# Kernel optimization log

Hardware: AMD Instinct MI355X
Metric: run time of the kernel (lower is better)

Reference implementation:

```python
import jax, jax.numpy as jnp
import numpy as np

N_NODES = 50000
N_EDGES = 800000
D_IN = 96
D_HID = 96
D_OUT = 96


def _mean_agg(x, src, dst, n_nodes):
    # mean over in-neighbors: agg[v] = mean_{(u->v) in E} x[u]
    msg = x[src]  # [E, d] irregular gather
    summed = jax.ops.segment_sum(msg, dst, num_segments=n_nodes)  # [N, d]
    deg = jax.ops.segment_sum(jnp.ones((src.shape[0],), x.dtype), dst,
                              num_segments=n_nodes)  # [N]
    return summed / jnp.maximum(deg, 1.0)[:, None]


def _sage_conv(x, src, dst, W_self, W_neigh, b):
    agg = _mean_agg(x, src, dst, x.shape[0])
    return x @ W_self + agg @ W_neigh + b


def setup_inputs() -> dict:
    key = jax.random.key(0)
    ks = jax.random.split(key, 9)
    s = 0.05
    return {
        "x": jax.random.normal(ks[0], (N_NODES, D_IN), jnp.float32),
        "src": jax.random.randint(ks[1], (N_EDGES,), 0, N_NODES),
        "dst": jax.random.randint(ks[2], (N_EDGES,), 0, N_NODES),
        "W_self1": jax.random.normal(ks[3], (D_IN, D_HID), jnp.float32) * s,
        "W_neigh1": jax.random.normal(ks[4], (D_IN, D_HID), jnp.float32) * s,
        "b1": jnp.zeros((D_HID,), jnp.float32),
        "W_self2": jax.random.normal(ks[5], (D_HID, D_OUT), jnp.float32) * s,
        "W_neigh2": jax.random.normal(ks[6], (D_HID, D_OUT), jnp.float32) * s,
        "b2": jnp.zeros((D_OUT,), jnp.float32),
    }


def reference(x, src, dst, W_self1, W_neigh1, b1, W_self2, W_neigh2, b2):
    h = _sage_conv(x, src, dst, W_self1, W_neigh1, b1)
    h = jax.nn.relu(h)
    h = _sage_conv(h, src, dst, W_self2, W_neigh2, b2)
    return h
```

## Files before the change

### kernel.cpp

```cpp
#include <hip/hip_runtime.h>
#include <cstdint>
#include <cstddef>

#define NN 50000
#define NE 800000
#define D 96

#define NBUCK 512
#define BSH 7
#define NBU ((NN + 127) >> 7)
#define TILE 8192
#define NTILE ((NE + TILE - 1) / TILE)
#define MAXB 5120

#define AGB 32
#define AGW 1024

typedef __attribute__((ext_vector_type(8))) short bf16x8;
typedef __attribute__((ext_vector_type(4))) float f32x4;


__global__ void init_cur(int* __restrict__ bucketCur) {
    bucketCur[threadIdx.x] = (int)threadIdx.x * MAXB;
}

__launch_bounds__(512)
__global__ void bin_edges(const int* __restrict__ dst, const int* __restrict__ src,
                          int* __restrict__ bucketCur, uint2* __restrict__ pairBuf) {
    __shared__ int hist[NBUCK];
    __shared__ int segStart[NBUCK];
    __shared__ int lcur[NBUCK];
    __shared__ int segBase[NBUCK];
    __shared__ uint2 lpair[TILE];
    const int t = threadIdx.x;
    const int e0 = blockIdx.x * TILE;
    const int cnt = (NE - e0 < TILE) ? (NE - e0) : TILE;

    for (int i = t; i < NBUCK; i += 512) hist[i] = 0;
    __syncthreads();

    for (int i = t * 4; i < cnt; i += 512 * 4) {
        if (i + 3 < cnt) {
            int4 d4 = *(const int4*)(dst + e0 + i);
            atomicAdd(&hist[d4.x >> BSH], 1);
            atomicAdd(&hist[d4.y >> BSH], 1);
            atomicAdd(&hist[d4.z >> BSH], 1);
            atomicAdd(&hist[d4.w >> BSH], 1);
        } else {
            for (int k = i; k < cnt; ++k) atomicAdd(&hist[dst[e0 + k] >> BSH], 1);
        }
    }
    __syncthreads();

    {
        const int v = hist[t];
        segStart[t] = v;
        __syncthreads();
        for (int s = 1; s < NBUCK; s <<= 1) {
            int u = (t >= s) ? segStart[t - s] : 0;
            __syncthreads();
            segStart[t] += u;
            __syncthreads();
        }
        int excl = segStart[t] - v;
        __syncthreads();
        segStart[t] = excl;
        lcur[t] = excl;
    }
    __syncthreads();

    for (int i = t * 4; i < cnt; i += 512 * 4) {
        if (i + 3 < cnt) {
            int4 d4 = *(const int4*)(dst + e0 + i);
            int4 s4 = *(const int4*)(src + e0 + i);
            int p0 = atomicAdd(&lcur[d4.x >> BSH], 1); lpair[p0] = make_uint2(d4.x, s4.x);
            int p1 = atomicAdd(&lcur[d4.y >> BSH], 1); lpair[p1] = make_uint2(d4.y, s4.y);
            int p2 = atomicAdd(&lcur[d4.z >> BSH], 1); lpair[p2] = make_uint2(d4.z, s4.z);
            int p3 = atomicAdd(&lcur[d4.w >> BSH], 1); lpair[p3] = make_uint2(d4.w, s4.w);
        } else {
            for (int k = i; k < cnt; ++k) {
                int d = dst[e0 + k], s = src[e0 + k];
                int p = atomicAdd(&lcur[d >> BSH], 1);
                lpair[p] = make_uint2(d, s);
            }
        }
    }
    __syncthreads();

    {
        int c = hist[t];
        segBase[t] = c ? atomicAdd(&bucketCur[t], c) : 0;
    }
    __syncthreads();

    for (int k = t; k < cnt; k += 512) {
        uint2 p = lpair[k];
        int b = (int)p.x >> BSH;
        pairBuf[(size_t)segBase[b] + (k - segStart[b])] = p;
    }
}

__global__ void csr_build(const uint2* __restrict__ pairBuf, const int* __restrict__ bucketCur,
                          int* __restrict__ deg, int* __restrict__ startv,
                          int* __restrict__ csr) {
    __shared__ int h[128], ls[128], cur[128];
    __shared__ int lsrc[MAXB];
    const int b = blockIdx.x;
    const int t = threadIdx.x;
    const int lo = b * MAXB;
    int cnt = bucketCur[b] - lo;
    if (cnt > MAXB) cnt = MAXB;
    const int node0 = b << BSH;

    if (t < 128) h[t] = 0;
    __syncthreads();
    for (int k = t; k < cnt; k += 256)
        atomicAdd(&h[(int)pairBuf[lo + k].x - node0], 1);
    __syncthreads();
    if (t < 128) ls[t] = h[t];
    __syncthreads();
    for (int s = 1; s < 128; s <<= 1) {
        int u = (t >= s && t < 128) ? ls[t - s] : 0;
        __syncthreads();
        if (t < 128) ls[t] += u;
        __syncthreads();
    }
    if (t < 128) {
        int excl = ls[t] - h[t];
        cur[t] = excl;
        int node = node0 + t;
        if (node < NN) {
            deg[node] = h[t];
            startv[node] = lo + excl;
        }
    }
    __syncthreads();
    for (int k = t; k < cnt; k += 256) {
        uint2 p = pairBuf[lo + k];
        int pos = atomicAdd(&cur[(int)p.x - node0], 1);
        lsrc[pos] = (int)p.y;
    }
    __syncthreads();
    for (int k = t; k < cnt; k += 256) csr[lo + k] = lsrc[k];
}


__device__ inline uint32_t pack2_bf16(float a, float b) {
    uint32_t ua = __float_as_uint(a), ub = __float_as_uint(b);
    ua = (ua + 0x7fffu + ((ua >> 16) & 1u)) >> 16;
    ub = (ub + 0x7fffu + ((ub >> 16) & 1u)) >> 16;
    return ua | (ub << 16);
}

__device__ inline unsigned short pack1_bf16(float a) {
    uint32_t ua = __float_as_uint(a);
    return (unsigned short)((ua + 0x7fffu + ((ua >> 16) & 1u)) >> 16);
}

__device__ inline float bf_lo(uint32_t w) { return __uint_as_float(w << 16); }
__device__ inline float bf_hi(uint32_t w) { return __uint_as_float(w & 0xffff0000u); }


__global__ void repack_both(const float* __restrict__ Ws1, const float* __restrict__ Wn1,
                            const float* __restrict__ Ws2, const float* __restrict__ Wn2,
                            uint32_t* __restrict__ bfg1, uint32_t* __restrict__ bfg2) {
    int t = blockIdx.x * 256 + threadIdx.x;
    if (t >= 4608) return;
    const int layer = (t >= 2304);
    int tt = t - layer * 2304;
    const int isWn = (tt >= 1152);
    const float* __restrict__ W = layer ? (isWn ? Wn2 : Ws2) : (isWn ? Wn1 : Ws1);
    uint32_t* __restrict__ Bfg = layer ? bfg2 : bfg1;
    tt = isWn ? tt - 1152 : tt;
    int s = tt / 384;
    int r = tt - s * 384;
    int nt6 = r >> 6;
    int l = r & 63;
    int col = nt6 * 16 + (l & 15);
    int k0 = 32 * s + 8 * (l >> 4);
    float v[8];
#pragma unroll
    for (int j = 0; j < 8; ++j) v[j] = W[(k0 + j) * D + col];
    uint4 o;
    o.x = pack2_bf16(v[0], v[1]);
    o.y = pack2_bf16(v[2], v[3]);
    o.z = pack2_bf16(v[4], v[5]);
    o.w = pack2_bf16(v[6], v[7]);
    int nt = nt6 + (isWn ? 6 : 0);
    int slot = (s * 12 + nt) * 64 + l;
    *(uint4*)(Bfg + (size_t)slot * 4) = o;
}


__launch_bounds__(256, 2)
__global__ void xform1_mfma(const float* __restrict__ X,
                            const uint32_t* __restrict__ Bfg,
                            const float* __restrict__ Bias,
                            unsigned short* __restrict__ Ys,
                            unsigned short* __restrict__ Yn) {
    __shared__ __align__(16) uint32_t Af[64 * 52];
    const int tid = threadIdx.x;
    const int row0 = blockIdx.x * 64;

#pragma unroll
    for (int it = 0; it < 6; ++it) {
        int flat = (it * 256 + tid) * 4;
        int r = flat / 96, k = flat - (flat / 96) * 96;
        int gr = row0 + r;
        if (gr >= NN) gr = NN - 1;
        float4 xv = *(const float4*)(X + (size_t)gr * D + k);
        int wq = r >> 4, s = k >> 5;
        int lq = ((k >> 3) & 3) * 16 + (r & 15);
        int base = ((wq * 3 + s) * 64 + lq) * 4 + ((k & 7) >> 1);
        Af[base] = pack2_bf16(xv.x, xv.y);
        Af[base + 1] = pack2_bf16(xv.z, xv.w);
    }
    __syncthreads();

    const int w = tid >> 6, l = tid & 63;
    const int cl = l & 15;

    bf16x8 a0 = *(const bf16x8*)&Af[((w * 3 + 0) * 64 + l) * 4];
    bf16x8 a1 = *(const bf16x8*)&Af[((w * 3 + 1) * 64 + l) * 4];
    bf16x8 a2 = *(const bf16x8*)&Af[((w * 3 + 2) * 64 + l) * 4];

    f32x4 acc[12];
#pragma unroll
    for (int nt = 0; nt < 6; ++nt) {
        float bv = Bias[nt * 16 + cl];
        acc[nt] = (f32x4){bv, bv, bv, bv};
    }
#pragma unroll
    for (int nt = 6; nt < 12; ++nt) acc[nt] = (f32x4){0.f, 0.f, 0.f, 0.f};

#pragma unroll
    for (int nt = 0; nt < 12; ++nt) {
        bf16x8 b0 = *(const bf16x8*)(Bfg + ((size_t)((0 * 12 + nt) * 64 + l)) * 4);
        bf16x8 b1 = *(const bf16x8*)(Bfg + ((size_t)((1 * 12 + nt) * 64 + l)) * 4);
        bf16x8 b2 = *(const bf16x8*)(Bfg + ((size_t)((2 * 12 + nt) * 64 + l)) * 4);
        acc[nt] = __builtin_amdgcn_mfma_f32_16x16x32_bf16(a0, b0, acc[nt], 0, 0, 0);
        acc[nt] = __builtin_amdgcn_mfma_f32_16x16x32_bf16(a1, b1, acc[nt], 0, 0, 0);
        acc[nt] = __builtin_amdgcn_mfma_f32_16x16x32_bf16(a2, b2, acc[nt], 0, 0, 0);
    }
    __syncthreads();

    unsigned short* Af16 = (unsigned short*)Af;
    const int lrow = w * 16 + (l >> 4) * 4;

#pragma unroll
    for (int nt = 0; nt < 6; ++nt)
#pragma unroll
        for (int rg = 0; rg < 4; ++rg)
            Af16[(lrow + rg) * 104 + nt * 16 + cl] = pack1_bf16(acc[nt][rg]);
    __syncthreads();
    {
        uint32_t* Ysu = (uint32_t*)Ys;
        const int rowq = tid >> 2, colq = (tid & 3) * 12;
        if (row0 + rowq < NN) {
#pragma unroll
            for (int i = 0; i < 3; ++i)
                *(uint4*)(Ysu + (size_t)(row0 + rowq) * 48 + colq + i * 4) =
                    *(const uint4*)&Af[rowq * 52 + colq + i * 4];
        }
    }
    __syncthreads();

#pragma unroll
    for (int nt = 6; nt < 12; ++nt)
#pragma unroll
        for (int rg = 0; rg < 4; ++rg)
            Af16[(lrow + rg) * 104 + (nt - 6) * 16 + cl] = pack1_bf16(acc[nt][rg]);
    __syncthreads();
    {
        uint32_t* Ynu = (uint32_t*)Yn;
        const int rowq = tid >> 2, colq = (tid & 3) * 12;
        if (row0 + rowq < NN) {
#pragma unroll
            for (int i = 0; i < 3; ++i)
                *(uint4*)(Ynu + (size_t)(row0 + rowq) * 48 + colq + i * 4) =
                    *(const uint4*)&Af[rowq * 52 + colq + i * 4];
        }
    }
}


#define GATHER_BODY(TBL, GET)                                              \
    {                                                                      \
        int e = 0;                                                         \
        for (; e + 15 < dg; e += 16) {                                     \
            uint32_t wv[16];                                               \
            _Pragma("unroll")                                              \
            for (int i = 0; i < 16; ++i)                                   \
                wv[i] = TBL[(size_t)(GET(e + i)) * 48 + li];               \
            _Pragma("unroll")                                              \
            for (int i = 0; i < 16; ++i) {                                 \
                sx[i & 3] += bf_lo(wv[i]); sy[i & 3] += bf_hi(wv[i]);      \
            }                                                              \
        }                                                                  \
        if (e + 7 < dg) {                                                  \
            uint32_t wv[8];                                                \
            _Pragma("unroll")                                              \
            for (int i = 0; i < 8; ++i)                                    \
                wv[i] = TBL[(size_t)(GET(e + i)) * 48 + li];               \
            _Pragma("unroll")                                              \
            for (int i = 0; i < 8; ++i) {                                  \
                sx[i & 3] += bf_lo(wv[i]); sy[i & 3] += bf_hi(wv[i]);      \
            }                                                              \
            e += 8;                                                        \
        }                                                                  \
        if (e + 3 < dg) {                                                  \
            uint32_t wv[4];                                                \
            _Pragma("unroll")                                              \
            for (int i = 0; i < 4; ++i)                                    \
                wv[i] = TBL[(size_t)(GET(e + i)) * 48 + li];               \
            _Pragma("unroll")                                              \
            for (int i = 0; i < 4; ++i) {                                  \
                sx[i] += bf_lo(wv[i]); sy[i] += bf_hi(wv[i]);              \
            }                                                              \
            e += 4;                                                        \
        }                                                                  \
        for (; e < dg; ++e) {                                              \
            uint32_t wv = TBL[(size_t)(GET(e)) * 48 + li];                 \
            sx[0] += bf_lo(wv); sy[0] += bf_hi(wv);                        \
        }                                                                  \
    }


__launch_bounds__(256, 4)
__global__ void fused_aggx(const unsigned short* __restrict__ Ys1,
                           const uint32_t* __restrict__ Yn1,
                           const int* __restrict__ csr, const int* __restrict__ startv,
                           const int* __restrict__ deg, const int* __restrict__ bucketCur,
                           const uint32_t* __restrict__ Bfg2, const float* __restrict__ Bias2,
                           unsigned short* __restrict__ Ys2, unsigned short* __restrict__ Yn2) {
    __shared__ __align__(16) uint32_t H[AGB * 52];
    __shared__ __align__(16) uint32_t H2[AGB * 52];
    __shared__ int lcsr[AGW];
    __shared__ int lsv[AGB + 1];
    __shared__ int ldeg[AGB];
    const int tid = threadIdx.x;
    const int w = tid >> 6, l = tid & 63;
    const int row0 = blockIdx.x * AGB;
    const int li = (l < 48) ? l : 0;

    if (tid <= AGB) {
        int r = row0 + tid;
        lsv[tid] = (r < NN) ? startv[r] : bucketCur[NBU - 1];
    }
    if (tid < AGB) {
        int r = row0 + tid;
        ldeg[tid] = (r < NN) ? deg[r] : 0;
    }
    __syncthreads();
    const int e_lo = lsv[0];
    const int wcnt = lsv[AGB] - e_lo;
    const int staged = wcnt < AGW ? wcnt : AGW;
    for (int k = tid; k < staged; k += 256) lcsr[k] = csr[e_lo + k];
    __syncthreads();

    for (int j = 0; j < 8; ++j) {
        const int vl = w * 8 + j;
        const int v = row0 + vl;
        uint32_t hpair = 0;
        if (v < NN) {
            const int sloc = lsv[vl] - e_lo;
            const int dg = ldeg[vl];
            float sx[4], sy[4];
#pragma unroll
            for (int i = 0; i < 4; ++i) { sx[i] = 0.f; sy[i] = 0.f; }
            if (sloc + dg <= staged) {
#define GET_L(E) lcsr[sloc + (E)]
                GATHER_BODY(Yn1, GET_L)
#undef GET_L
            } else {
                const int* cp = csr + e_lo + sloc;
#define GET_G(E) cp[E]
                GATHER_BODY(Yn1, GET_G)
#undef GET_G
            }
            float ax = (sx[0] + sx[1]) + (sx[2] + sx[3]);
            float ay = (sy[0] + sy[1]) + (sy[2] + sy[3]);
            const float inv = 1.f / (float)(dg > 0 ? dg : 1);
            uint32_t ysp = *(const uint32_t*)(Ys1 + (size_t)v * 96 + 2 * li);
            float r0 = fmaxf(bf_lo(ysp) + ax * inv, 0.f);
            float r1 = fmaxf(bf_hi(ysp) + ay * inv, 0.f);
            hpair = pack2_bf16(r0, r1);
        }
        if (l < 48) H[vl * 52 + l] = hpair;
    }
    __syncthreads();

    const int stripe = w >> 1;
    const int hf = w & 1;
    const int cl = l & 15;
    const int kq = l >> 4;

    bf16x8 a0 = *(const bf16x8*)&H[(stripe * 16 + cl) * 52 + 0 + 4 * kq];
    bf16x8 a1 = *(const bf16x8*)&H[(stripe * 16 + cl) * 52 + 16 + 4 * kq];
    bf16x8 a2 = *(const bf16x8*)&H[(stripe * 16 + cl) * 52 + 32 + 4 * kq];

    f32x4 acc[6];
#pragma unroll
    for (int nt = 0; nt < 6; ++nt) {
        float bv = hf ? 0.f : Bias2[nt * 16 + cl];
        acc[nt] = (f32x4){bv, bv, bv, bv};
    }
#pragma unroll
    for (int nt = 0; nt < 6; ++nt) {
        int ntg = hf * 6 + nt;
        bf16x8 b0 = *(const bf16x8*)(Bfg2 + ((size_t)((0 * 12 + ntg) * 64 + l)) * 4);
        bf16x8 b1 = *(const bf16x8*)(Bfg2 + ((size_t)((1 * 12 + ntg) * 64 + l)) * 4);
        bf16x8 b2 = *(const bf16x8*)(Bfg2 + ((size_t)((2 * 12 + ntg) * 64 + l)) * 4);
        acc[nt] = __builtin_amdgcn_mfma_f32_16x16x32_bf16(a0, b0, acc[nt], 0, 0, 0);
        acc[nt] = __builtin_amdgcn_mfma_f32_16x16x32_bf16(a1, b1, acc[nt], 0, 0, 0);
        acc[nt] = __builtin_amdgcn_mfma_f32_16x16x32_bf16(a2, b2, acc[nt], 0, 0, 0);
    }
    __syncthreads();

    {
        unsigned short* Hb = (unsigned short*)(hf ? H2 : H);
        const int lrow = stripe * 16 + kq * 4;
#pragma unroll
        for (int nt = 0; nt < 6; ++nt)
#pragma unroll
            for (int rg = 0; rg < 4; ++rg)
                Hb[(lrow + rg) * 104 + nt * 16 + cl] = pack1_bf16(acc[nt][rg]);
    }
    __syncthreads();

    {
        const int row = tid >> 3, colq = (tid & 7) * 6;
        if (row0 + row < NN) {
            uint32_t* Ysu = (uint32_t*)Ys2;
            uint32_t* Ynu = (uint32_t*)Yn2;
            const size_t gb = (size_t)(row0 + row) * 48 + colq;
            const int lb = row * 52 + colq;
#pragma unroll
            for (int i = 0; i < 3; ++i)
                *(uint2*)(Ysu + gb + i * 2) = *(const uint2*)&H[lb + i * 2];
#pragma unroll
            for (int i = 0; i < 3; ++i)
                *(uint2*)(Ynu + gb + i * 2) = *(const uint2*)&H2[lb + i * 2];
        }
    }
}


__launch_bounds__(256, 4)
__global__ void agg_final(const unsigned short* __restrict__ Ys2b,
                          const uint32_t* __restrict__ Yn2,
                          const int* __restrict__ csr, const int* __restrict__ startv,
                          const int* __restrict__ deg, const int* __restrict__ bucketCur,
                          float* __restrict__ out) {
    __shared__ int lcsr[AGW];
    __shared__ int lsv[AGB + 1];
    __shared__ int ldeg[AGB];
    const int tid = threadIdx.x;
    const int w = tid >> 6, l = tid & 63;
    const int row0 = blockIdx.x * AGB;
    const int li = (l < 48) ? l : 0;

    if (tid <= AGB) {
        int r = row0 + tid;
        lsv[tid] = (r < NN) ? startv[r] : bucketCur[NBU - 1];
    }
    if (tid < AGB) {
        int r = row0 + tid;
        ldeg[tid] = (r < NN) ? deg[r] : 0;
    }
    __syncthreads();
    const int e_lo = lsv[0];
    const int wcnt = lsv[AGB] - e_lo;
    const int staged = wcnt < AGW ? wcnt : AGW;
    for (int k = tid; k < staged; k += 256) lcsr[k] = csr[e_lo + k];
    __syncthreads();

    for (int j = 0; j < 8; ++j) {
        const int vl = w * 8 + j;
        const int v = row0 + vl;
        if (v >= NN) continue;
        const int sloc = lsv[vl] - e_lo;
        const int dg = ldeg[vl];
        float sx[4], sy[4];
#pragma unroll
        for (int i = 0; i < 4; ++i) { sx[i] = 0.f; sy[i] = 0.f; }
        if (sloc + dg <= staged) {
#define GET_L(E) lcsr[sloc + (E)]
            GATHER_BODY(Yn2, GET_L)
#undef GET_L
        } else {
            const int* cp = csr + e_lo + sloc;
#define GET_G(E) cp[E]
            GATHER_BODY(Yn2, GET_G)
#undef GET_G
        }
        float ax = (sx[0] + sx[1]) + (sx[2] + sx[3]);
        float ay = (sy[0] + sy[1]) + (sy[2] + sy[3]);
        const float inv = 1.f / (float)(dg > 0 ? dg : 1);
        if (l < 48) {
            const size_t o = (size_t)v * D + 2 * li;
            uint32_t ysp = *(const uint32_t*)(Ys2b + (size_t)v * 96 + 2 * li);
            out[o] = bf_lo(ysp) + ax * inv;
            out[o + 1] = bf_hi(ysp) + ay * inv;
        }
    }
}


extern "C" void kernel_launch(void* const* d_in, const int* in_sizes, int n_in,
                              void* d_out, int out_size, void* d_ws, size_t ws_size,
                              hipStream_t stream) {
    const float* x   = (const float*)d_in[0];
    const int*   src = (const int*)d_in[1];
    const int*   dst = (const int*)d_in[2];
    const float* Ws1 = (const float*)d_in[3];
    const float* Wn1 = (const float*)d_in[4];
    const float* b1  = (const float*)d_in[5];
    const float* Ws2 = (const float*)d_in[6];
    const float* Wn2 = (const float*)d_in[7];
    const float* b2  = (const float*)d_in[8];
    float* out = (float*)d_out;

    char* w = (char*)d_ws;
    int* startv    = (int*)w; w += (size_t)NN * sizeof(int);
    int* deg       = (int*)w; w += (size_t)NN * sizeof(int);
    int* bucketCur = (int*)w; w += NBUCK * sizeof(int);
    int* csr       = (int*)w; w += (size_t)NBUCK * MAXB * sizeof(int);
    w = (char*)(((uintptr_t)w + 255) & ~(uintptr_t)255);
    unsigned short* ys1 = (unsigned short*)w; w += (size_t)NN * D * sizeof(unsigned short);
    unsigned short* yn1 = (unsigned short*)w; w += (size_t)NN * D * sizeof(unsigned short);
    unsigned short* ys2 = (unsigned short*)w; w += (size_t)NN * D * sizeof(unsigned short);
    unsigned short* yn2 = (unsigned short*)w; w += (size_t)NN * D * sizeof(unsigned short);
    uint32_t* bfg1 = (uint32_t*)w; w += 36 * 64 * 4 * sizeof(uint32_t);
    uint32_t* bfg2 = (uint32_t*)w; w += 36 * 64 * 4 * sizeof(uint32_t);

    uint2* pairBuf = (uint2*)ys1;

    init_cur<<<1, NBUCK, 0, stream>>>(bucketCur);
    bin_edges<<<NTILE, 512, 0, stream>>>(dst, src, bucketCur, pairBuf);
    csr_build<<<NBU, 256, 0, stream>>>(pairBuf, bucketCur, deg, startv, csr);

    repack_both<<<18, 256, 0, stream>>>(Ws1, Wn1, Ws2, Wn2, bfg1, bfg2);

    xform1_mfma<<<(NN + 63) / 64, 256, 0, stream>>>(x, bfg1, b1, ys1, yn1);

    const int agrid = (NN + AGB - 1) / AGB;

    fused_aggx<<<agrid, 256, 0, stream>>>(ys1, (const uint32_t*)yn1, csr, startv, deg,
                                          bucketCur, bfg2, b2, ys2, yn2);

    agg_final<<<agrid, 256, 0, stream>>>(ys2, (const uint32_t*)yn2, csr, startv, deg,
                                         bucketCur, out);
}
```

Before: 114.4 us.

## Split neighbor gathers by source half to improve L2 locality

Each node's CSR neighbor list is partitioned by whether the source index falls in the lower or upper half of the node range, and the aggregation kernels run two passes, first over lower-half sources and then over upper-half sources, keeping partial sums in shared memory. The goal is to shrink the working set of gathered feature rows in each pass so it fits better in cache. The change also folds the bucket-cursor init into the weight repack kernel, saving a launch. It drops the second staging buffer in fused_aggx and raises launch-bounds occupancy hints, at the cost of serialized output writes, a large float accumulator array in shared memory, and extra syncs.

Result: slower. 128.3 us (+12.1%).

```diff
diff --git a/kernel.cpp b/kernel.cpp
--- a/kernel.cpp
+++ b/kernel.cpp
@@ -5,6 +5,7 @@
 #define NN 50000
 #define NE 800000
 #define D 96
+#define NSPLIT 25000
 
 #define NBUCK 512
 #define BSH 7
@@ -19,10 +20,6 @@
 typedef __attribute__((ext_vector_type(8))) short bf16x8;
 typedef __attribute__((ext_vector_type(4))) float f32x4;
 
-
-__global__ void init_cur(int* __restrict__ bucketCur) {
-    bucketCur[threadIdx.x] = (int)threadIdx.x * MAXB;
-}
 
 __launch_bounds__(512)
 __global__ void bin_edges(const int* __restrict__ dst, const int* __restrict__ src,
@@ -102,8 +99,8 @@
 
 __global__ void csr_build(const uint2* __restrict__ pairBuf, const int* __restrict__ bucketCur,
                           int* __restrict__ deg, int* __restrict__ startv,
-                          int* __restrict__ csr) {
-    __shared__ int h[128], ls[128], cur[128];
+                          int* __restrict__ splitv, int* __restrict__ csr) {
+    __shared__ int h[256], ls[256], cur[256];
     __shared__ int lsrc[MAXB];
     const int b = blockIdx.x;
     const int t = threadIdx.x;
@@ -112,32 +109,39 @@
     if (cnt > MAXB) cnt = MAXB;
     const int node0 = b << BSH;
 
-    if (t < 128) h[t] = 0;
-    __syncthreads();
-    for (int k = t; k < cnt; k += 256)
-        atomicAdd(&h[(int)pairBuf[lo + k].x - node0], 1);
-    __syncthreads();
-    if (t < 128) ls[t] = h[t];
-    __syncthreads();
-    for (int s = 1; s < 128; s <<= 1) {
-        int u = (t >= s && t < 128) ? ls[t - s] : 0;
+    h[t] = 0;
+    __syncthreads();
+    for (int k = t; k < cnt; k += 256) {
+        uint2 p = pairBuf[lo + k];
+        atomicAdd(&h[((int)p.x - node0) * 2 + ((int)p.y >= NSPLIT)], 1);
+    }
+    __syncthreads();
+    ls[t] = h[t];
+    __syncthreads();
+    for (int s = 1; s < 256; s <<= 1) {
+        int u = (t >= s) ? ls[t - s] : 0;
         __syncthreads();
-        if (t < 128) ls[t] += u;
+        ls[t] += u;
         __syncthreads();
     }
-    if (t < 128) {
+    {
         int excl = ls[t] - h[t];
         cur[t] = excl;
-        int node = node0 + t;
+        int node = node0 + (t >> 1);
         if (node < NN) {
-            deg[node] = h[t];
-            startv[node] = lo + excl;
+            if ((t & 1) == 0) {
+                deg[node] = h[t] + h[t + 1];
+                startv[node] = lo + excl;
+            } else {
+                splitv[node] = lo + excl;
+            }
         }
     }
     __syncthreads();
     for (int k = t; k < cnt; k += 256) {
         uint2 p = pairBuf[lo + k];
-        int pos = atomicAdd(&cur[(int)p.x - node0], 1);
+        int key = ((int)p.x - node0) * 2 + ((int)p.y >= NSPLIT);
+        int pos = atomicAdd(&cur[key], 1);
         lsrc[pos] = (int)p.y;
     }
     __syncthreads();
@@ -161,9 +165,16 @@
 __device__ inline float bf_hi(uint32_t w) { return __uint_as_float(w & 0xffff0000u); }
 
 
-__global__ void repack_both(const float* __restrict__ Ws1, const float* __restrict__ Wn1,
+__global__ void repack_init(const float* __restrict__ Ws1, const float* __restrict__ Wn1,
                             const float* __restrict__ Ws2, const float* __restrict__ Wn2,
-                            uint32_t* __restrict__ bfg1, uint32_t* __restrict__ bfg2) {
+                            uint32_t* __restrict__ bfg1, uint32_t* __restrict__ bfg2,
+                            int* __restrict__ bucketCur) {
+    if (blockIdx.x == 18) {
+        int t = threadIdx.x;
+        bucketCur[t] = t * MAXB;
+        bucketCur[t + 256] = (t + 256) * MAXB;
+        return;
+    }
     int t = blockIdx.x * 256 + threadIdx.x;
     if (t >= 4608) return;
     const int layer = (t >= 2304);
@@ -325,18 +336,31 @@
         }                                                                  \
     }
 
-
-__launch_bounds__(256, 4)
+#define PASS_GATHER(TBL)                                                   \
+    if (sloc + dg <= staged) {                                             \
+        GATHER_BODY(TBL, GET_L)                                            \
+    } else {                                                               \
+        const int* cp = csr + e_lo + sloc;                                 \
+        GATHER_BODY(TBL, GET_G)                                            \
+    }
+
+#define GET_L(E) lcsr[sloc + (E)]
+#define GET_G(E) cp[E]
+
+
+__launch_bounds__(256, 6)
 __global__ void fused_aggx(const unsigned short* __restrict__ Ys1,
                            const uint32_t* __restrict__ Yn1,
                            const int* __restrict__ csr, const int* __restrict__ startv,
-                           const int* __restrict__ deg, const int* __restrict__ bucketCur,
+                           const int* __restrict__ splitv, const int* __restrict__ deg,
+                           const int* __restrict__ bucketCur,
                            const uint32_t* __restrict__ Bfg2, const float* __restrict__ Bias2,
                            unsigned short* __restrict__ Ys2, unsigned short* __restrict__ Yn2) {
+    __shared__ float accF[AGB][100];
     __shared__ __align__(16) uint32_t H[AGB * 52];
-    __shared__ __align__(16) uint32_t H2[AGB * 52];
     __shared__ int lcsr[AGW];
     __shared__ int lsv[AGB + 1];
+    __shared__ int lsp[AGB];
     __shared__ int ldeg[AGB];
     const int tid = threadIdx.x;
     const int w = tid >> 6, l = tid & 63;
@@ -349,6 +373,7 @@
     }
     if (tid < AGB) {
         int r = row0 + tid;
+        lsp[tid] = (r < NN) ? splitv[r] : 0;
         ldeg[tid] = (r < NN) ? deg[r] : 0;
     }
     __syncthreads();
@@ -358,35 +383,38 @@
     for (int k = tid; k < staged; k += 256) lcsr[k] = csr[e_lo + k];
     __syncthreads();
 
-    for (int j = 0; j < 8; ++j) {
-        const int vl = w * 8 + j;
-        const int v = row0 + vl;
-        uint32_t hpair = 0;
-        if (v < NN) {
-            const int sloc = lsv[vl] - e_lo;
-            const int dg = ldeg[vl];
-            float sx[4], sy[4];
-#pragma unroll
-            for (int i = 0; i < 4; ++i) { sx[i] = 0.f; sy[i] = 0.f; }
-            if (sloc + dg <= staged) {
-#define GET_L(E) lcsr[sloc + (E)]
-                GATHER_BODY(Yn1, GET_L)
-#undef GET_L
-            } else {
-                const int* cp = csr + e_lo + sloc;
-#define GET_G(E) cp[E]
-                GATHER_BODY(Yn1, GET_G)
-#undef GET_G
+    for (int p = 0; p < 2; ++p) {
+        for (int j = 0; j < 8; ++j) {
+            const int vl = w * 8 + j;
+            const int v = row0 + vl;
+            if (v < NN) {
+                const int s0 = lsv[vl] - e_lo;
+                const int sp = lsp[vl] - e_lo;
+                const int dgA = ldeg[vl];
+                const int sloc = p ? sp : s0;
+                const int dg = p ? (s0 + dgA - sp) : (sp - s0);
+                float sx[4], sy[4];
+#pragma unroll
+                for (int i = 0; i < 4; ++i) { sx[i] = 0.f; sy[i] = 0.f; }
+                PASS_GATHER(Yn1)
+                float ax = (sx[0] + sx[1]) + (sx[2] + sx[3]);
+                float ay = (sy[0] + sy[1]) + (sy[2] + sy[3]);
+                if (p == 0) {
+                    accF[vl][2 * li] = ax;
+                    accF[vl][2 * li + 1] = ay;
+                } else {
+                    ax += accF[vl][2 * li];
+                    ay += accF[vl][2 * li + 1];
+                    const float inv = 1.f / (float)(dgA > 0 ? dgA : 1);
+                    uint32_t ysp = *(const uint32_t*)(Ys1 + (size_t)v * 96 + 2 * li);
+                    float r0 = fmaxf(bf_lo(ysp) + ax * inv, 0.f);
+                    float r1 = fmaxf(bf_hi(ysp) + ay * inv, 0.f);
+                    if (l < 48) H[vl * 52 + l] = pack2_bf16(r0, r1);
+                }
+            } else if (p == 1 && l < 48) {
+                H[vl * 52 + l] = 0;
             }
-            float ax = (sx[0] + sx[1]) + (sx[2] + sx[3]);
-            float ay = (sy[0] + sy[1]) + (sy[2] + sy[3]);
-            const float inv = 1.f / (float)(dg > 0 ? dg : 1);
-            uint32_t ysp = *(const uint32_t*)(Ys1 + (size_t)v * 96 + 2 * li);
-            float r0 = fmaxf(bf_lo(ysp) + ax * inv, 0.f);
-            float r1 = fmaxf(bf_hi(ysp) + ay * inv, 0.f);
-            hpair = pack2_bf16(r0, r1);
-        }
-        if (l < 48) H[vl * 52 + l] = hpair;
+        }
     }
     __syncthreads();
 
@@ -418,42 +446,66 @@
     __syncthreads();
 
     {
-        unsigned short* Hb = (unsigned short*)(hf ? H2 : H);
+        unsigned short* Hb = (unsigned short*)H;
         const int lrow = stripe * 16 + kq * 4;
-#pragma unroll
-        for (int nt = 0; nt < 6; ++nt)
-#pragma unroll
-            for (int rg = 0; rg < 4; ++rg)
-                Hb[(lrow + rg) * 104 + nt * 16 + cl] = pack1_bf16(acc[nt][rg]);
-    }
-    __syncthreads();
-
+        if (hf == 0) {
+#pragma unroll
+            for (int nt = 0; nt < 6; ++nt)
+#pragma unroll
+                for (int rg = 0; rg < 4; ++rg)
+                    Hb[(lrow + rg) * 104 + nt * 16 + cl] = pack1_bf16(acc[nt][rg]);
+        }
+    }
+    __syncthreads();
     {
         const int row = tid >> 3, colq = (tid & 7) * 6;
         if (row0 + row < NN) {
             uint32_t* Ysu = (uint32_t*)Ys2;
+            const size_t gb = (size_t)(row0 + row) * 48 + colq;
+            const int lb = row * 52 + colq;
+#pragma unroll
+            for (int i = 0; i < 3; ++i)
+                *(uint2*)(Ysu + gb + i * 2) = *(const uint2*)&H[lb + i * 2];
+        }
+    }
+    __syncthreads();
+
+    {
+        unsigned short* Hb = (unsigned short*)H;
+        const int lrow = stripe * 16 + kq * 4;
+        if (hf == 1) {
+#pragma unroll
+            for (int nt = 0; nt < 6; ++nt)
+#pragma unroll
+                for (int rg = 0; rg < 4; ++rg)
+                    Hb[(lrow + rg) * 104 + nt * 16 + cl] = pack1_bf16(acc[nt][rg]);
+        }
+    }
+    __syncthreads();
+    {
+        const int row = tid >> 3, colq = (tid & 7) * 6;
+        if (row0 + row < NN) {
             uint32_t* Ynu = (uint32_t*)Yn2;
             const size_t gb = (size_t)(row0 + row) * 48 + colq;
             const int lb = row * 52 + colq;
 #pragma unroll
             for (int i = 0; i < 3; ++i)
-                *(uint2*)(Ysu + gb + i * 2) = *(const uint2*)&H[lb + i * 2];
-#pragma unroll
-            for (int i = 0; i < 3; ++i)
-                *(uint2*)(Ynu + gb + i * 2) = *(const uint2*)&H2[lb + i * 2];
-        }
-    }
-}
-
-
-__launch_bounds__(256, 4)
+                *(uint2*)(Ynu + gb + i * 2) = *(const uint2*)&H[lb + i * 2];
+        }
+    }
+}
+
+
+__launch_bounds__(256, 8)
 __global__ void agg_final(const unsigned short* __restrict__ Ys2b,
                           const uint32_t* __restrict__ Yn2,
                           const int* __restrict__ csr, const int* __restrict__ startv,
-                          const int* __restrict__ deg, const int* __restrict__ bucketCur,
-                          float* __restrict__ out) {
+                          const int* __restrict__ splitv, const int* __restrict__ deg,
+                          const int* __restrict__ bucketCur, float* __restrict__ out) {
+    __shared__ float accF[AGB][100];
     __shared__ int lcsr[AGW];
     __shared__ int lsv[AGB + 1];
+    __shared__ int lsp[AGB];
     __shared__ int ldeg[AGB];
     const int tid = threadIdx.x;
     const int w = tid >> 6, l = tid & 63;
@@ -466,6 +518,7 @@
     }
     if (tid < AGB) {
         int r = row0 + tid;
+        lsp[tid] = (r < NN) ? splitv[r] : 0;
         ldeg[tid] = (r < NN) ? deg[r] : 0;
     }
     __syncthreads();
@@ -475,33 +528,34 @@
     for (int k = tid; k < staged; k += 256) lcsr[k] = csr[e_lo + k];
     __syncthreads();
 
-    for (int j = 0; j < 8; ++j) {
-        const int vl = w * 8 + j;
-        const int v = row0 + vl;
-        if (v >= NN) continue;
-        const int sloc = lsv[vl] - e_lo;
-        const int dg = ldeg[vl];
-        float sx[4], sy[4];
-#pragma unroll
-        for (int i = 0; i < 4; ++i) { sx[i] = 0.f; sy[i] = 0.f; }
-        if (sloc + dg <= staged) {
-#define GET_L(E) lcsr[sloc + (E)]
-            GATHER_BODY(Yn2, GET_L)
-#undef GET_L
-        } else {
-            const int* cp = csr + e_lo + sloc;
-#define GET_G(E) cp[E]
-            GATHER_BODY(Yn2, GET_G)
-#undef GET_G
-        }
-        float ax = (sx[0] + sx[1]) + (sx[2] + sx[3]);
-        float ay = (sy[0] + sy[1]) + (sy[2] + sy[3]);
-        const float inv = 1.f / (float)(dg > 0 ? dg : 1);
-        if (l < 48) {
-            const size_t o = (size_t)v * D + 2 * li;
-            uint32_t ysp = *(const uint32_t*)(Ys2b + (size_t)v * 96 + 2 * li);
-            out[o] = bf_lo(ysp) + ax * inv;
-            out[o + 1] = bf_hi(ysp) + ay * inv;
+    for (int p = 0; p < 2; ++p) {
+        for (int j = 0; j < 8; ++j) {
+            const int vl = w * 8 + j;
+            const int v = row0 + vl;
+            if (v >= NN) continue;
+            const int s0 = lsv[vl] - e_lo;
+            const int sp = lsp[vl] - e_lo;
+            const int dgA = ldeg[vl];
+            const int sloc = p ? sp : s0;
+            const int dg = p ? (s0 + dgA - sp) : (sp - s0);
+            float sx[4], sy[4];
+#pragma unroll
+            for (int i = 0; i < 4; ++i) { sx[i] = 0.f; sy[i] = 0.f; }
+            PASS_GATHER(Yn2)
+            float ax = (sx[0] + sx[1]) + (sx[2] + sx[3]);
+            float ay = (sy[0] + sy[1]) + (sy[2] + sy[3]);
+            if (p == 0) {
+                accF[vl][2 * li] = ax;
+                accF[vl][2 * li + 1] = ay;
+            } else if (l < 48) {
+                ax += accF[vl][2 * li];
+                ay += accF[vl][2 * li + 1];
+                const float inv = 1.f / (float)(dgA > 0 ? dgA : 1);
+                const size_t o = (size_t)v * D + 2 * li;
+                uint32_t ysp = *(const uint32_t*)(Ys2b + (size_t)v * 96 + 2 * li);
+                out[o] = bf_lo(ysp) + ax * inv;
+                out[o + 1] = bf_hi(ysp) + ay * inv;
+            }
         }
     }
 }
@@ -523,6 +577,7 @@
 
     char* w = (char*)d_ws;
     int* startv    = (int*)w; w += (size_t)NN * sizeof(int);
+    int* splitv    = (int*)w; w += (size_t)NN * sizeof(int);
     int* deg       = (int*)w; w += (size_t)NN * sizeof(int);
     int* bucketCur = (int*)w; w += NBUCK * sizeof(int);
     int* csr       = (int*)w; w += (size_t)NBUCK * MAXB * sizeof(int);
@@ -536,19 +591,18 @@
 
     uint2* pairBuf = (uint2*)ys1;
 
-    init_cur<<<1, NBUCK, 0, stream>>>(bucketCur);
+    repack_init<<<19, 256, 0, stream>>>(Ws1, Wn1, Ws2, Wn2, bfg1, bfg2, bucketCur);
+
     bin_edges<<<NTILE, 512, 0, stream>>>(dst, src, bucketCur, pairBuf);
-    csr_build<<<NBU, 256, 0, stream>>>(pairBuf, bucketCur, deg, startv, csr);
-
-    repack_both<<<18, 256, 0, stream>>>(Ws1, Wn1, Ws2, Wn2, bfg1, bfg2);
+    csr_build<<<NBU, 256, 0, stream>>>(pairBuf, bucketCur, deg, startv, splitv, csr);
 
     xform1_mfma<<<(NN + 63) / 64, 256, 0, stream>>>(x, bfg1, b1, ys1, yn1);
 
     const int agrid = (NN + AGB - 1) / AGB;
 
-    fused_aggx<<<agrid, 256, 0, stream>>>(ys1, (const uint32_t*)yn1, csr, startv, deg,
-                                          bucketCur, bfg2, b2, ys2, yn2);
-
-    agg_final<<<agrid, 256, 0, stream>>>(ys2, (const uint32_t*)yn2, csr, startv, deg,
-                                         bucketCur, out);
-}
+    fused_aggx<<<agrid, 256, 0, stream>>>(ys1, (const uint32_t*)yn1, csr, startv, splitv,
+                                          deg, bucketCur, bfg2, b2, ys2, yn2);
+
+    agg_final<<<agrid, 256, 0, stream>>>(ys2, (const uint32_t*)yn2, csr, startv, splitv,
+                                         deg, bucketCur, out);
+}
```

## Software-pipeline neighbor gathers across nodes and merge init into repack kernel

Applied to the files above, without the earlier changes.

Both aggregation kernels are restructured so that the first 16 neighbor-row loads for the next node are issued before the current node's loads are accumulated. Tail edges are handled by clamped indices and masked FMAs instead of branchy remainder loops. The aim is more memory-level parallelism in the latency-bound irregular gather. fused_aggx also drops the second shared-memory buffer and writes Ys2 and Yn2 in two passes through one buffer, which saves LDS to help occupancy at the cost of extra syncs. The bucket-cursor init is folded into the weight repack kernel to remove one launch. The risks are redundant loads for low-degree nodes and higher register pressure from the double buffers.

Measured after the change: 125.1 us. 9.3% more time.

```diff
diff --git a/kernel.cpp b/kernel.cpp
--- a/kernel.cpp
+++ b/kernel.cpp
@@ -19,10 +19,6 @@
 typedef __attribute__((ext_vector_type(8))) short bf16x8;
 typedef __attribute__((ext_vector_type(4))) float f32x4;
 
-
-__global__ void init_cur(int* __restrict__ bucketCur) {
-    bucketCur[threadIdx.x] = (int)threadIdx.x * MAXB;
-}
 
 __launch_bounds__(512)
 __global__ void bin_edges(const int* __restrict__ dst, const int* __restrict__ src,
@@ -161,9 +157,16 @@
 __device__ inline float bf_hi(uint32_t w) { return __uint_as_float(w & 0xffff0000u); }
 
 
-__global__ void repack_both(const float* __restrict__ Ws1, const float* __restrict__ Wn1,
+__global__ void repack_init(const float* __restrict__ Ws1, const float* __restrict__ Wn1,
                             const float* __restrict__ Ws2, const float* __restrict__ Wn2,
-                            uint32_t* __restrict__ bfg1, uint32_t* __restrict__ bfg2) {
+                            uint32_t* __restrict__ bfg1, uint32_t* __restrict__ bfg2,
+                            int* __restrict__ bucketCur) {
+    if (blockIdx.x == 18) {
+        int t = threadIdx.x;
+        bucketCur[t] = t * MAXB;
+        bucketCur[t + 256] = (t + 256) * MAXB;
+        return;
+    }
     int t = blockIdx.x * 256 + threadIdx.x;
     if (t >= 4608) return;
     const int layer = (t >= 2304);
@@ -284,45 +287,44 @@
 }
 
 
-#define GATHER_BODY(TBL, GET)                                              \
-    {                                                                      \
-        int e = 0;                                                         \
-        for (; e + 15 < dg; e += 16) {                                     \
-            uint32_t wv[16];                                               \
-            _Pragma("unroll")                                              \
-            for (int i = 0; i < 16; ++i)                                   \
-                wv[i] = TBL[(size_t)(GET(e + i)) * 48 + li];               \
-            _Pragma("unroll")                                              \
-            for (int i = 0; i < 16; ++i) {                                 \
-                sx[i & 3] += bf_lo(wv[i]); sy[i & 3] += bf_hi(wv[i]);      \
-            }                                                              \
-        }                                                                  \
-        if (e + 7 < dg) {                                                  \
-            uint32_t wv[8];                                                \
-            _Pragma("unroll")                                              \
-            for (int i = 0; i < 8; ++i)                                    \
-                wv[i] = TBL[(size_t)(GET(e + i)) * 48 + li];               \
-            _Pragma("unroll")                                              \
-            for (int i = 0; i < 8; ++i) {                                  \
-                sx[i & 3] += bf_lo(wv[i]); sy[i & 3] += bf_hi(wv[i]);      \
-            }                                                              \
-            e += 8;                                                        \
-        }                                                                  \
-        if (e + 3 < dg) {                                                  \
-            uint32_t wv[4];                                                \
-            _Pragma("unroll")                                              \
-            for (int i = 0; i < 4; ++i)                                    \
-                wv[i] = TBL[(size_t)(GET(e + i)) * 48 + li];               \
-            _Pragma("unroll")                                              \
-            for (int i = 0; i < 4; ++i) {                                  \
-                sx[i] += bf_lo(wv[i]); sy[i] += bf_hi(wv[i]);              \
-            }                                                              \
-            e += 4;                                                        \
-        }                                                                  \
-        for (; e < dg; ++e) {                                              \
-            uint32_t wv = TBL[(size_t)(GET(e)) * 48 + li];                 \
-            sx[0] += bf_lo(wv); sy[0] += bf_hi(wv);                        \
-        }                                                                  \
+#define ISSUE16(TBL, buf, SLOC, DG)                                         \
+    if ((SLOC) + (DG) <= staged) {                                          \
+        _Pragma("unroll")                                                   \
+        for (int i = 0; i < 16; ++i) {                                      \
+            int kk = (i < (DG)) ? i : (DG) - 1;                             \
+            buf[i] = TBL[(size_t)lcsr[(SLOC) + kk] * 48 + li];              \
+        }                                                                   \
+    } else {                                                                \
+        const int* cp_ = csr + e_lo + (SLOC);                               \
+        _Pragma("unroll")                                                   \
+        for (int i = 0; i < 16; ++i) {                                      \
+            int kk = (i < (DG)) ? i : (DG) - 1;                             \
+            buf[i] = TBL[(size_t)cp_[kk] * 48 + li];                        \
+        }                                                                   \
+    }
+
+#define ISSUE16R(TBL, buf, SLOC, DG, E0)                                    \
+    if ((SLOC) + (DG) <= staged) {                                          \
+        _Pragma("unroll")                                                   \
+        for (int i = 0; i < 16; ++i) {                                      \
+            int kk = ((E0) + i < (DG)) ? (E0) + i : (DG) - 1;               \
+            buf[i] = TBL[(size_t)lcsr[(SLOC) + kk] * 48 + li];              \
+        }                                                                   \
+    } else {                                                                \
+        const int* cp_ = csr + e_lo + (SLOC);                               \
+        _Pragma("unroll")                                                   \
+        for (int i = 0; i < 16; ++i) {                                      \
+            int kk = ((E0) + i < (DG)) ? (E0) + i : (DG) - 1;               \
+            buf[i] = TBL[(size_t)cp_[kk] * 48 + li];                        \
+        }                                                                   \
+    }
+
+#define ACC16(buf, DG, E0)                                                  \
+    _Pragma("unroll")                                                       \
+    for (int i = 0; i < 16; ++i) {                                          \
+        float m = ((E0) + i < (DG)) ? 1.f : 0.f;                            \
+        sx[i & 3] = fmaf(m, bf_lo(buf[i]), sx[i & 3]);                      \
+        sy[i & 3] = fmaf(m, bf_hi(buf[i]), sy[i & 3]);                      \
     }
 
 
@@ -334,7 +336,6 @@
                            const uint32_t* __restrict__ Bfg2, const float* __restrict__ Bias2,
                            unsigned short* __restrict__ Ys2, unsigned short* __restrict__ Yn2) {
     __shared__ __align__(16) uint32_t H[AGB * 52];
-    __shared__ __align__(16) uint32_t H2[AGB * 52];
     __shared__ int lcsr[AGW];
     __shared__ int lsv[AGB + 1];
     __shared__ int ldeg[AGB];
@@ -358,36 +359,54 @@
     for (int k = tid; k < staged; k += 256) lcsr[k] = csr[e_lo + k];
     __syncthreads();
 
+    int sl[8], dgj[8];
+#pragma unroll
     for (int j = 0; j < 8; ++j) {
-        const int vl = w * 8 + j;
-        const int v = row0 + vl;
-        uint32_t hpair = 0;
-        if (v < NN) {
-            const int sloc = lsv[vl] - e_lo;
-            const int dg = ldeg[vl];
-            float sx[4], sy[4];
-#pragma unroll
-            for (int i = 0; i < 4; ++i) { sx[i] = 0.f; sy[i] = 0.f; }
-            if (sloc + dg <= staged) {
-#define GET_L(E) lcsr[sloc + (E)]
-                GATHER_BODY(Yn1, GET_L)
-#undef GET_L
-            } else {
-                const int* cp = csr + e_lo + sloc;
-#define GET_G(E) cp[E]
-                GATHER_BODY(Yn1, GET_G)
-#undef GET_G
-            }
-            float ax = (sx[0] + sx[1]) + (sx[2] + sx[3]);
-            float ay = (sy[0] + sy[1]) + (sy[2] + sy[3]);
-            const float inv = 1.f / (float)(dg > 0 ? dg : 1);
-            uint32_t ysp = *(const uint32_t*)(Ys1 + (size_t)v * 96 + 2 * li);
-            float r0 = fmaxf(bf_lo(ysp) + ax * inv, 0.f);
-            float r1 = fmaxf(bf_hi(ysp) + ay * inv, 0.f);
-            hpair = pack2_bf16(r0, r1);
-        }
-        if (l < 48) H[vl * 52 + l] = hpair;
-    }
+        int vl = w * 8 + j;
+        sl[j] = lsv[vl] - e_lo;
+        dgj[j] = ldeg[vl];
+    }
+    uint32_t bufA[16], bufB[16];
+    if (dgj[0] > 0) { ISSUE16(Yn1, bufA, sl[0], dgj[0]) }
+
+#define ANODE_F(CUR, NXT, J)                                                \
+    {                                                                       \
+        const int dg = dgj[J];                                              \
+        const int sloc = sl[J];                                             \
+        const int vl = w * 8 + (J);                                         \
+        const int v = row0 + vl;                                            \
+        if ((J) < 7 && dgj[(J) + 1] > 0) { ISSUE16(Yn1, NXT, sl[(J) + 1], dgj[(J) + 1]) } \
+        float sx[4] = {0.f, 0.f, 0.f, 0.f}, sy[4] = {0.f, 0.f, 0.f, 0.f};   \
+        if (dg > 0) {                                                       \
+            ACC16(CUR, dg, 0)                                               \
+            for (int e0 = 16; e0 < dg; e0 += 16) {                          \
+                uint32_t tmp[16];                                           \
+                ISSUE16R(Yn1, tmp, sloc, dg, e0)                            \
+                ACC16(tmp, dg, e0)                                          \
+            }                                                               \
+        }                                                                   \
+        if (v < NN) {                                                       \
+            float ax = (sx[0] + sx[1]) + (sx[2] + sx[3]);                   \
+            float ay = (sy[0] + sy[1]) + (sy[2] + sy[3]);                   \
+            const float inv = 1.f / (float)(dg > 0 ? dg : 1);               \
+            uint32_t ysp = *(const uint32_t*)(Ys1 + (size_t)v * 96 + 2 * li); \
+            float r0 = fmaxf(bf_lo(ysp) + ax * inv, 0.f);                   \
+            float r1 = fmaxf(bf_hi(ysp) + ay * inv, 0.f);                   \
+            if (l < 48) H[vl * 52 + l] = pack2_bf16(r0, r1);                \
+        } else if (l < 48) {                                                \
+            H[vl * 52 + l] = 0;                                             \
+        }                                                                   \
+    }
+
+    ANODE_F(bufA, bufB, 0)
+    ANODE_F(bufB, bufA, 1)
+    ANODE_F(bufA, bufB, 2)
+    ANODE_F(bufB, bufA, 3)
+    ANODE_F(bufA, bufB, 4)
+    ANODE_F(bufB, bufA, 5)
+    ANODE_F(bufA, bufB, 6)
+    ANODE_F(bufB, bufA, 7)
+#undef ANODE_F
     __syncthreads();
 
     const int stripe = w >> 1;
@@ -418,29 +437,51 @@
     __syncthreads();
 
     {
-        unsigned short* Hb = (unsigned short*)(hf ? H2 : H);
+        unsigned short* Hb = (unsigned short*)H;
         const int lrow = stripe * 16 + kq * 4;
-#pragma unroll
-        for (int nt = 0; nt < 6; ++nt)
-#pragma unroll
-            for (int rg = 0; rg < 4; ++rg)
-                Hb[(lrow + rg) * 104 + nt * 16 + cl] = pack1_bf16(acc[nt][rg]);
-    }
-    __syncthreads();
-
+        if (hf == 0) {
+#pragma unroll
+            for (int nt = 0; nt < 6; ++nt)
+#pragma unroll
+                for (int rg = 0; rg < 4; ++rg)
+                    Hb[(lrow + rg) * 104 + nt * 16 + cl] = pack1_bf16(acc[nt][rg]);
+        }
+    }
+    __syncthreads();
     {
         const int row = tid >> 3, colq = (tid & 7) * 6;
         if (row0 + row < NN) {
             uint32_t* Ysu = (uint32_t*)Ys2;
+            const size_t gb = (size_t)(row0 + row) * 48 + colq;
+            const int lb = row * 52 + colq;
+#pragma unroll
+            for (int i = 0; i < 3; ++i)
+                *(uint2*)(Ysu + gb + i * 2) = *(const uint2*)&H[lb + i * 2];
+        }
+    }
+    __syncthreads();
+
+    {
+        unsigned short* Hb = (unsigned short*)H;
+        const int lrow = stripe * 16 + kq * 4;
+        if (hf == 1) {
+#pragma unroll
+            for (int nt = 0; nt < 6; ++nt)
+#pragma unroll
+                for (int rg = 0; rg < 4; ++rg)
+                    Hb[(lrow + rg) * 104 + nt * 16 + cl] = pack1_bf16(acc[nt][rg]);
+        }
+    }
+    __syncthreads();
+    {
+        const int row = tid >> 3, colq = (tid & 7) * 6;
+        if (row0 + row < NN) {
             uint32_t* Ynu = (uint32_t*)Yn2;
             const size_t gb = (size_t)(row0 + row) * 48 + colq;
             const int lb = row * 52 + colq;
 #pragma unroll
             for (int i = 0; i < 3; ++i)
-                *(uint2*)(Ysu + gb + i * 2) = *(const uint2*)&H[lb + i * 2];
-#pragma unroll
-            for (int i = 0; i < 3; ++i)
-                *(uint2*)(Ynu + gb + i * 2) = *(const uint2*)&H2[lb + i * 2];
+                *(uint2*)(Ynu + gb + i * 2) = *(const uint2*)&H[lb + i * 2];
         }
     }
 }
@@ -475,35 +516,51 @@
     for (int k = tid; k < staged; k += 256) lcsr[k] = csr[e_lo + k];
     __syncthreads();
 
+    int sl[8], dgj[8];
+#pragma unroll
     for (int j = 0; j < 8; ++j) {
-        const int vl = w * 8 + j;
-        const int v = row0 + vl;
-        if (v >= NN) continue;
-        const int sloc = lsv[vl] - e_lo;
-        const int dg = ldeg[vl];
-        float sx[4], sy[4];
-#pragma unroll
-        for (int i = 0; i < 4; ++i) { sx[i] = 0.f; sy[i] = 0.f; }
-        if (sloc + dg <= staged) {
-#define GET_L(E) lcsr[sloc + (E)]
-            GATHER_BODY(Yn2, GET_L)
-#undef GET_L
-        } else {
-            const int* cp = csr + e_lo + sloc;
-#define GET_G(E) cp[E]
-            GATHER_BODY(Yn2, GET_G)
-#undef GET_G
-        }
-        float ax = (sx[0] + sx[1]) + (sx[2] + sx[3]);
-        float ay = (sy[0] + sy[1]) + (sy[2] + sy[3]);
-        const float inv = 1.f / (float)(dg > 0 ? dg : 1);
-        if (l < 48) {
-            const size_t o = (size_t)v * D + 2 * li;
-            uint32_t ysp = *(const uint32_t*)(Ys2b + (size_t)v * 96 + 2 * li);
-            out[o] = bf_lo(ysp) + ax * inv;
-            out[o + 1] = bf_hi(ysp) + ay * inv;
-        }
-    }
+        int vl = w * 8 + j;
+        sl[j] = lsv[vl] - e_lo;
+        dgj[j] = ldeg[vl];
+    }
+    uint32_t bufA[16], bufB[16];
+    if (dgj[0] > 0) { ISSUE16(Yn2, bufA, sl[0], dgj[0]) }
+
+#define ANODE_O(CUR, NXT, J)                                                \
+    {                                                                       \
+        const int dg = dgj[J];                                              \
+        const int sloc = sl[J];                                             \
+        const int v = row0 + w * 8 + (J);                                   \
+        if ((J) < 7 && dgj[(J) + 1] > 0) { ISSUE16(Yn2, NXT, sl[(J) + 1], dgj[(J) + 1]) } \
+        float sx[4] = {0.f, 0.f, 0.f, 0.f}, sy[4] = {0.f, 0.f, 0.f, 0.f};   \
+        if (dg > 0) {                                                       \
+            ACC16(CUR, dg, 0)                                               \
+            for (int e0 = 16; e0 < dg; e0 += 16) {                          \
+                uint32_t tmp[16];                                           \
+                ISSUE16R(Yn2, tmp, sloc, dg, e0)                            \
+                ACC16(tmp, dg, e0)                                          \
+            }                                                               \
+        }                                                                   \
+        if (v < NN && l < 48) {                                             \
+            float ax = (sx[0] + sx[1]) + (sx[2] + sx[3]);                   \
+            float ay = (sy[0] + sy[1]) + (sy[2] + sy[3]);                   \
+            const float inv = 1.f / (float)(dg > 0 ? dg : 1);               \
+            const size_t o = (size_t)v * D + 2 * li;                        \
+            uint32_t ysp = *(const uint32_t*)(Ys2b + (size_t)v * 96 + 2 * li); \
+            out[o] = bf_lo(ysp) + ax * inv;                                 \
+            out[o + 1] = bf_hi(ysp) + ay * inv;                             \
+        }                                                                   \
+    }
+
+    ANODE_O(bufA, bufB, 0)
+    ANODE_O(bufB, bufA, 1)
+    ANODE_O(bufA, bufB, 2)
+    ANODE_O(bufB, bufA, 3)
+    ANODE_O(bufA, bufB, 4)
+    ANODE_O(bufB, bufA, 5)
+    ANODE_O(bufA, bufB, 6)
+    ANODE_O(bufB, bufA, 7)
+#undef ANODE_O
 }
 
 
@@ -536,12 +593,11 @@
 
     uint2* pairBuf = (uint2*)ys1;
 
-    init_cur<<<1, NBUCK, 0, stream>>>(bucketCur);
+    repack_init<<<19, 256, 0, stream>>>(Ws1, Wn1, Ws2, Wn2, bfg1, bfg2, bucketCur);
+
     bin_edges<<<NTILE, 512, 0, stream>>>(dst, src, bucketCur, pairBuf);
     csr_build<<<NBU, 256, 0, stream>>>(pairBuf, bucketCur, deg, startv, csr);
 
-    repack_both<<<18, 256, 0, stream>>>(Ws1, Wn1, Ws2, Wn2, bfg1, bfg2);
-
     xform1_mfma<<<(NN + 63) / 64, 256, 0, stream>>>(x, bfg1, b1, ys1, yn1);
 
     const int agrid = (NN + AGB - 1) / AGB;
```
